# Kernel optimization log

Hardware: AMD Instinct MI355X
Metric: run time of the kernel (lower is better)

The kernel has to match this reference:

```python
import jax, jax.numpy as jnp
import numpy as np

# snntorch Leaky defaults / CFG constants
BETA = 0.9      # CFG.lif_beta
IAPP = 0.0      # CFG.Iapp
THR = 1.0       # snn.Leaky default threshold
SLOPE = 25.0    # surrogate.fast_sigmoid default slope


@jax.custom_vjp
def spike(x):
    # Heaviside spike with fast-sigmoid surrogate gradient
    return (x > 0).astype(x.dtype)

def _spike_fwd(x):
    return spike(x), x

def _spike_bwd(x, g):
    return (g / (SLOPE * jnp.abs(x) + 1.0) ** 2,)

spike.defvjp(_spike_fwd, _spike_bwd)


def setup_inputs() -> dict:
    key = jax.random.key(0)
    z = jax.random.normal(key, (32, 1024, 512), dtype=jnp.float32)
    return {"z": z}


def reference(z):
    # z: [B, T, H]; sequential LIF over time axis.
    # snntorch Leaky (reset='subtract'):
    #   reset = detach(V_prev > thr)
    #   V_k   = beta * V_prev + input_k - reset * thr
    #   spk_k = heaviside(V_k - thr)
    # Original loop: input at step k is z[:, k-1] + Iapp (noise std = 0.0).
    B, T, H = z.shape
    zt = jnp.transpose(z[:, :-1, :], (1, 0, 2))  # [T-1, B, H]
    V0 = jnp.zeros((B, H), dtype=z.dtype)

    def step(V, zin):
        reset = jax.lax.stop_gradient((V > THR).astype(V.dtype))
        Vn = BETA * V + (zin + IAPP) - reset * THR
        spk = spike(Vn - THR)
        return Vn, spk

    _, spks = jax.lax.scan(step, V0, zt)  # spks: [T-1, B, H]
    # T[:, 0, :] stays zero (loop starts at k=1)
    Tout = jnp.concatenate(
        [jnp.zeros((B, 1, H), dtype=z.dtype), jnp.transpose(spks, (1, 0, 2))],
        axis=1,
    )
    return Tout
```

## Files before the change

### kernel.cpp

```cpp
#include <hip/hip_runtime.h>


#define LIF_H 512
#define LIF_T 1024
#define CH 128
#define NCH 8
#define NPROD 4
#define NTHREADS (64 * (1 + NPROD))

__global__ __launch_bounds__(NTHREADS, 1) void lif_kernel(const float* __restrict__ z,
                                                          float* __restrict__ out) {
    __shared__ float lds[2][CH * 64];

    const int tid  = threadIdx.x;
    const int wave = tid >> 6;
    const int lane = tid & 63;
    const int bid  = blockIdx.x;
    const int b    = bid >> 3;
    const int h0   = (bid & 7) << 6;

    const float* zb = z   + b * (LIF_T * LIF_H) + h0;
    float*       ob = out + b * (LIF_T * LIF_H) + h0;

    if (wave == 0) {
        ob[lane] = 0.0f;
    } else {
        const int p = wave - 1;
#pragma unroll
        for (int j = 0; j < 8; ++j) {
            const int r0 = p * 32 + j * 4;
            const float* g = zb + (r0 + (lane >> 4)) * LIF_H + (lane & 15) * 4;
            __builtin_amdgcn_global_load_lds(
                (__attribute__((address_space(1))) void*)g,
                (__attribute__((address_space(3))) void*)&lds[0][r0 * 64],
                16, 0, 0);
        }
        asm volatile("s_waitcnt vmcnt(0)" ::: "memory");
    }
    asm volatile("" ::: "memory");
    __builtin_amdgcn_s_barrier();
    asm volatile("" ::: "memory");

    float V = 0.0f;

    for (int c = 0; c < NCH; ++c) {
        const int cur = c & 1;

        if (wave > 0) {
            if (c + 1 < NCH) {
                const int p = wave - 1;
#pragma unroll
                for (int j = 0; j < 8; ++j) {
                    const int r0 = p * 32 + j * 4;
                    const float* g = zb + ((c + 1) * CH + r0 + (lane >> 4)) * LIF_H
                                        + (lane & 15) * 4;
                    __builtin_amdgcn_global_load_lds(
                        (__attribute__((address_space(1))) void*)g,
                        (__attribute__((address_space(3))) void*)&lds[cur ^ 1][r0 * 64],
                        16, 0, 0);
                }
                asm volatile("s_waitcnt vmcnt(0)" ::: "memory");
            }
        } else {
            const float* lb = &lds[cur][0];
            const bool lastc = (c == NCH - 1);
#pragma unroll 1
            for (int sub = 0; sub < 4; ++sub) {
                float rb[32];
#pragma unroll
                for (int i = 0; i < 32; ++i)
                    rb[i] = lb[(sub * 32 + i) * 64 + lane];
                __builtin_amdgcn_sched_barrier(0);

                const int s0 = c * CH + sub * 32;
                if (!lastc || sub < 3) {
#pragma unroll
                    for (int i = 0; i < 32; ++i) {
                        const float v0 = __fadd_rn(__fmul_rn(0.9f, V), rb[i]);
                        const float Vn = (V > 1.0f) ? __fsub_rn(v0, 1.0f) : v0;
                        ob[(s0 + i + 1) * LIF_H + lane] = (Vn > 1.0f) ? 1.0f : 0.0f;
                        V = Vn;
                    }
                } else {
#pragma unroll
                    for (int i = 0; i < 31; ++i) {
                        const float v0 = __fadd_rn(__fmul_rn(0.9f, V), rb[i]);
                        const float Vn = (V > 1.0f) ? __fsub_rn(v0, 1.0f) : v0;
                        ob[(s0 + i + 1) * LIF_H + lane] = (Vn > 1.0f) ? 1.0f : 0.0f;
                        V = Vn;
                    }
                }
                __builtin_amdgcn_sched_barrier(0);
            }
        }

        asm volatile("" ::: "memory");
        __builtin_amdgcn_s_barrier();
        asm volatile("" ::: "memory");
    }
}

extern "C" void kernel_launch(void* const* d_in, const int* in_sizes, int n_in,
                              void* d_out, int out_size, void* d_ws, size_t ws_size,
                              hipStream_t stream) {
    const float* z = (const float*)d_in[0];
    float* out = (float*)d_out;
    hipLaunchKernelGGL(lif_kernel, dim3(256), dim3(NTHREADS), 0, stream, z, out);
}
```

Measured before the change: 118.0 us.

## Triple-buffer LDS prefetch and double-buffer register loads in LIF recurrence

Switches from a double-buffered to a triple-buffered LDS ring held in dynamic shared memory, so producer waves prefetch two chunks ahead and wait with vmcnt(8) instead of draining every load. The consumer wave alternates between two register buffers, so LDS reads for the next sub-block overlap the current serial chain. The reset term now reuses the previous spike value rather than recomputing a compare, which shortens the dependent chain. The cost is more LDS (96KB) and higher register pressure.

```diff
diff --git a/kernel.cpp b/kernel.cpp
--- a/kernel.cpp
+++ b/kernel.cpp
@@ -8,9 +8,14 @@
 #define NPROD 4
 #define NTHREADS (64 * (1 + NPROD))
 
+#define GLDS(gptr, lptr)                                                     \
+    __builtin_amdgcn_global_load_lds(                                        \
+        (const __attribute__((address_space(1))) void*)(gptr),               \
+        (__attribute__((address_space(3))) void*)(lptr), 16, 0, 0)
+
 __global__ __launch_bounds__(NTHREADS, 1) void lif_kernel(const float* __restrict__ z,
                                                           float* __restrict__ out) {
-    __shared__ float lds[2][CH * 64];
+    extern __shared__ float lds[];
 
     const int tid  = threadIdx.x;
     const int wave = tid >> 6;
@@ -29,74 +34,82 @@
 #pragma unroll
         for (int j = 0; j < 8; ++j) {
             const int r0 = p * 32 + j * 4;
-            const float* g = zb + (r0 + (lane >> 4)) * LIF_H + (lane & 15) * 4;
-            __builtin_amdgcn_global_load_lds(
-                (__attribute__((address_space(1))) void*)g,
-                (__attribute__((address_space(3))) void*)&lds[0][r0 * 64],
-                16, 0, 0);
+            GLDS(zb + (r0 + (lane >> 4)) * LIF_H + (lane & 15) * 4,
+                 &lds[0 * (CH * 64) + r0 * 64]);
         }
-        asm volatile("s_waitcnt vmcnt(0)" ::: "memory");
+#pragma unroll
+        for (int j = 0; j < 8; ++j) {
+            const int r0 = p * 32 + j * 4;
+            GLDS(zb + (CH + r0 + (lane >> 4)) * LIF_H + (lane & 15) * 4,
+                 &lds[1 * (CH * 64) + r0 * 64]);
+        }
+        __builtin_amdgcn_sched_barrier(0);
+        asm volatile("s_waitcnt vmcnt(8)" ::: "memory");
     }
-    asm volatile("" ::: "memory");
     __builtin_amdgcn_s_barrier();
-    asm volatile("" ::: "memory");
 
     float V = 0.0f;
+    float r = 0.0f;
+    int cbuf = 0;
 
+#define LDRB(rb, sub)                                                        \
+    _Pragma("unroll")                                                        \
+    for (int i = 0; i < 32; ++i) rb[i] = lb[((sub) * 32 + i) * 64 + lane];
+
+#define CHAIN(rb, s0, N)                                                     \
+    _Pragma("unroll")                                                        \
+    for (int i = 0; i < (N); ++i) {                                          \
+        const float u  = __fadd_rn(__fmul_rn(0.9f, V), rb[i]);               \
+        const float Vn = __fsub_rn(u, r);                                    \
+        const float sp = (Vn > 1.0f) ? 1.0f : 0.0f;                          \
+        ob[((s0) + i + 1) * LIF_H + lane] = sp;                              \
+        r = sp;                                                              \
+        V = Vn;                                                              \
+    }
+
+#pragma unroll 1
     for (int c = 0; c < NCH; ++c) {
-        const int cur = c & 1;
-
         if (wave > 0) {
-            if (c + 1 < NCH) {
+            if (c + 2 < NCH) {
                 const int p = wave - 1;
+                int wbuf = cbuf + 2; if (wbuf >= 3) wbuf -= 3;
+                float* dst = &lds[wbuf * (CH * 64)];
+                const float* src = zb + (c + 2) * CH * LIF_H;
 #pragma unroll
                 for (int j = 0; j < 8; ++j) {
                     const int r0 = p * 32 + j * 4;
-                    const float* g = zb + ((c + 1) * CH + r0 + (lane >> 4)) * LIF_H
-                                        + (lane & 15) * 4;
-                    __builtin_amdgcn_global_load_lds(
-                        (__attribute__((address_space(1))) void*)g,
-                        (__attribute__((address_space(3))) void*)&lds[cur ^ 1][r0 * 64],
-                        16, 0, 0);
+                    GLDS(src + (r0 + (lane >> 4)) * LIF_H + (lane & 15) * 4,
+                         &dst[r0 * 64]);
                 }
+                __builtin_amdgcn_sched_barrier(0);
+                asm volatile("s_waitcnt vmcnt(8)" ::: "memory");
+            } else if (c + 1 < NCH) {
                 asm volatile("s_waitcnt vmcnt(0)" ::: "memory");
             }
         } else {
-            const float* lb = &lds[cur][0];
-            const bool lastc = (c == NCH - 1);
-#pragma unroll 1
-            for (int sub = 0; sub < 4; ++sub) {
-                float rb[32];
-#pragma unroll
-                for (int i = 0; i < 32; ++i)
-                    rb[i] = lb[(sub * 32 + i) * 64 + lane];
-                __builtin_amdgcn_sched_barrier(0);
-
-                const int s0 = c * CH + sub * 32;
-                if (!lastc || sub < 3) {
-#pragma unroll
-                    for (int i = 0; i < 32; ++i) {
-                        const float v0 = __fadd_rn(__fmul_rn(0.9f, V), rb[i]);
-                        const float Vn = (V > 1.0f) ? __fsub_rn(v0, 1.0f) : v0;
-                        ob[(s0 + i + 1) * LIF_H + lane] = (Vn > 1.0f) ? 1.0f : 0.0f;
-                        V = Vn;
-                    }
-                } else {
-#pragma unroll
-                    for (int i = 0; i < 31; ++i) {
-                        const float v0 = __fadd_rn(__fmul_rn(0.9f, V), rb[i]);
-                        const float Vn = (V > 1.0f) ? __fsub_rn(v0, 1.0f) : v0;
-                        ob[(s0 + i + 1) * LIF_H + lane] = (Vn > 1.0f) ? 1.0f : 0.0f;
-                        V = Vn;
-                    }
-                }
-                __builtin_amdgcn_sched_barrier(0);
+            const float* lb = &lds[cbuf * (CH * 64)];
+            const int s0 = c * CH;
+            float rbA[32], rbB[32];
+            LDRB(rbA, 0);
+            LDRB(rbB, 1);
+            __builtin_amdgcn_sched_barrier(0);
+            CHAIN(rbA, s0 + 0, 32);
+            LDRB(rbA, 2);
+            __builtin_amdgcn_sched_barrier(0);
+            CHAIN(rbB, s0 + 32, 32);
+            LDRB(rbB, 3);
+            __builtin_amdgcn_sched_barrier(0);
+            CHAIN(rbA, s0 + 64, 32);
+            __builtin_amdgcn_sched_barrier(0);
+            if (c < NCH - 1) {
+                CHAIN(rbB, s0 + 96, 32);
+            } else {
+                CHAIN(rbB, s0 + 96, 31);
             }
         }
 
-        asm volatile("" ::: "memory");
         __builtin_amdgcn_s_barrier();
-        asm volatile("" ::: "memory");
+        cbuf = (cbuf == 2) ? 0 : cbuf + 1;
     }
 }
 
@@ -105,5 +118,6 @@
                               hipStream_t stream) {
     const float* z = (const float*)d_in[0];
     float* out = (float*)d_out;
-    hipLaunchKernelGGL(lif_kernel, dim3(256), dim3(NTHREADS), 0, stream, z, out);
+    hipLaunchKernelGGL(lif_kernel, dim3(256), dim3(NTHREADS),
+                       3 * CH * 64 * sizeof(float), stream, z, out);
 }
```

Result: faster. 113.4 us (-3.9%).
